# Kernel optimization log

Measured on AMD Instinct MI355X. Metric: run time of the kernel, lower is better.

The kernel has to match this reference:

```python
import jax, jax.numpy as jnp
import numpy as np

B, T, C, H = 65536, 100, 7, 2  # batch, timesteps, covariates, lstm hidden


def setup_inputs() -> dict:
    key = jax.random.key(0)
    ks = iter(jax.random.split(key, 32))
    def rn(shape, s=0.1):
        return jax.random.normal(next(ks), shape, dtype=jnp.float32) * s
    inp = {"x": jax.random.normal(next(ks), (B, T, C), dtype=jnp.float32)}
    for l, din in ((0, C), (1, 2 * H)):
        for suf in ("", "r"):
            inp[f"w_ih_l{l}{suf}"] = rn((4 * H, din))
            inp[f"w_hh_l{l}{suf}"] = rn((4 * H, H))
            inp[f"b_ih_l{l}{suf}"] = rn((4 * H,))
            inp[f"b_hh_l{l}{suf}"] = rn((4 * H,))
    inp["fc1_w"] = rn((64, 4 * T))
    inp["fc1_b"] = rn((64,))
    inp["fc2_w"] = rn((20, 64))
    inp["fc2_b"] = rn((20,))
    return inp


def _lstm_dir(xw, w_hh, b_hh, reverse):
    # xw: [T, B, 4H] precomputed input projection (x @ W_ih.T + b_ih)
    if reverse:
        xw = xw[::-1]
    h0 = jnp.zeros((xw.shape[1], H), xw.dtype)
    c0 = jnp.zeros((xw.shape[1], H), xw.dtype)

    def step(carry, gx):
        h, c = carry
        g = gx + h @ w_hh.T + b_hh            # [B, 4H]
        i, f, gg, o = jnp.split(g, 4, axis=-1)  # torch gate order i,f,g,o
        c = jax.nn.sigmoid(f) * c + jax.nn.sigmoid(i) * jnp.tanh(gg)
        h = jax.nn.sigmoid(o) * jnp.tanh(c)
        return (h, c), h

    _, hs = jax.lax.scan(step, (h0, c0), xw)
    if reverse:
        hs = hs[::-1]
    return hs  # [T, B, H]


def _bilstm_layer(x_tbf, w_ih_f, w_hh_f, b_ih_f, b_hh_f,
                  w_ih_b, w_hh_b, b_ih_b, b_hh_b):
    xw_f = jnp.einsum('tbc,gc->tbg', x_tbf, w_ih_f) + b_ih_f
    xw_b = jnp.einsum('tbc,gc->tbg', x_tbf, w_ih_b) + b_ih_b
    hf = _lstm_dir(xw_f, w_hh_f, b_hh_f, False)
    hb = _lstm_dir(xw_b, w_hh_b, b_hh_b, True)
    return jnp.concatenate([hf, hb], axis=-1)  # [T, B, 2H]


def reference(x,
              w_ih_l0, w_hh_l0, b_ih_l0, b_hh_l0,
              w_ih_l0r, w_hh_l0r, b_ih_l0r, b_hh_l0r,
              w_ih_l1, w_hh_l1, b_ih_l1, b_hh_l1,
              w_ih_l1r, w_hh_l1r, b_ih_l1r, b_hh_l1r,
              fc1_w, fc1_b, fc2_w, fc2_b):
    xt = jnp.transpose(x.reshape(-1, T, C), (1, 0, 2))  # [T, B, C] time-major
    h1 = _bilstm_layer(xt, w_ih_l0, w_hh_l0, b_ih_l0, b_hh_l0,
                       w_ih_l0r, w_hh_l0r, b_ih_l0r, b_hh_l0r)
    h2 = _bilstm_layer(h1, w_ih_l1, w_hh_l1, b_ih_l1, b_hh_l1,
                       w_ih_l1r, w_hh_l1r, b_ih_l1r, b_hh_l1r)
    out = jnp.transpose(h2, (1, 0, 2)).reshape(-1, 4 * T)  # flatten [B, 4T]
    out = jax.nn.relu(out)                  # relu BEFORE fc1, as in original
    out = jax.nn.relu(out @ fc1_w.T + fc1_b)
    return out @ fc2_w.T + fc2_b            # [B, 20]
```

## Files before the change

### kernel.cpp

```cpp
#include <hip/hip_runtime.h>

#define Bn 65536
#define Tn 100
#define Cn 7

typedef short short8 __attribute__((ext_vector_type(8)));
typedef float float4v __attribute__((ext_vector_type(4)));

__device__ __forceinline__ float fast_rcp(float x) { return __builtin_amdgcn_rcpf(x); }
__device__ __forceinline__ float sig_f(float x) { return fast_rcp(1.f + __expf(-x)); }
__device__ __forceinline__ float tanh_f(float x) { return 1.f - 2.f * fast_rcp(__expf(2.f * x) + 1.f); }
__device__ __forceinline__ unsigned bf16rne(float x) {
    unsigned u = __float_as_uint(x);
    return (u + 0x7fffu + ((u >> 16) & 1u)) >> 16;
}
__device__ __forceinline__ float bf_lo(unsigned u) { return __uint_as_float(u << 16); }
__device__ __forceinline__ float bf_hi(unsigned u) { return __uint_as_float(u & 0xffff0000u); }

__device__ __forceinline__ float dpp_xor1(float x) {
    return __uint_as_float((unsigned)__builtin_amdgcn_mov_dpp(
        (int)__float_as_uint(x), 0xB1, 0xF, 0xF, true));
}

typedef const __attribute__((address_space(1))) void* gp_t;
typedef __attribute__((address_space(3))) void* sp_t;
__device__ __forceinline__ void async_copy_dw(const void* g, void* l) {
    __builtin_amdgcn_global_load_lds((gp_t)g, (sp_t)l, 4, 0, 0);
}

__global__ void w2prep_kernel(const float* __restrict__ fc1_w, unsigned short* __restrict__ w2g) {
    int idx = blockIdx.x * 256 + threadIdx.x;
    int w  = idx >> 12;
    int d  = (idx >> 11) & 1;
    int n  = (idx >> 5) & 63;
    int kk = idx & 31;
    int tt = kk >> 1, i = kk & 1;
    int t  = d ? (99 - 10 * w - tt) : (10 * w + tt);
    float v = (kk < 20) ? fc1_w[n * 400 + 4 * t + 2 * d + i] : 0.f;
    w2g[idx] = (unsigned short)bf16rne(v);
}

__global__ __launch_bounds__(256) void l0_kernel(
    const float* __restrict__ x,
    const float* __restrict__ wih_f, const float* __restrict__ whh_f,
    const float* __restrict__ bih_f, const float* __restrict__ bhh_f,
    const float* __restrict__ wih_r, const float* __restrict__ whh_r,
    const float* __restrict__ bih_r, const float* __restrict__ bhh_r,
    unsigned* __restrict__ h1u)
{
    __shared__ float xs[4][2][1120];

    const int tid  = threadIdx.x;
    const int wv   = tid >> 6;
    const int lane = tid & 63;
    const int rev  = wv >> 1;
    const int sgrp = wv & 1;
    const int cid  = lane & 1;
    const int s    = lane >> 1;
    const int b    = blockIdx.x * 64 + sgrp * 32 + s;

    const float* wih = rev ? wih_r : wih_f;
    const float* whh = rev ? whh_r : whh_f;
    const float* bih = rev ? bih_r : bih_f;
    const float* bhh = rev ? bhh_r : bhh_f;

    float wi[28], whA[4], whB[4], bias4[4];
#pragma unroll
    for (int j = 0; j < 4; ++j) {
        const int k = cid + 2 * j;
#pragma unroll
        for (int c = 0; c < 7; ++c) wi[j * 7 + c] = wih[k * 7 + c];
        whA[j] = whh[k * 2 + cid];
        whB[j] = whh[k * 2 + (cid ^ 1)];
        bias4[j] = bih[k] + bhh[k];
    }

    const int e  = (lane >= 35) ? 1 : 0;
    const int r0 = lane - 35 * e;
    const float* xsamp = x + (size_t)(blockIdx.x * 64 + sgrp * 32 + e) * 700;

    auto stage = [&](int ch, int p) {
        const int off = rev ? (665 - 35 * ch) : (35 * ch);
        const float* g = xsamp + off + r0;
        float* l = &xs[wv][p][lane];
        int r = r0;
#pragma unroll
        for (int i = 0; i < 17; ++i) {
            async_copy_dw(g, l);
            l += 64;
            const int c = (r >= 6) ? 1 : 0;
            g += c ? 1394 : 729;
            r += c ? -6 : 29;
        }
        if (lane < 32) async_copy_dw(g, l);
    };

    float hs = 0.f, ho = 0.f, cc = 0.f;

    stage(0, 0);
#pragma unroll 1
    for (int chk = 0; chk < 20; ++chk) {
        if (chk == 0) __builtin_amdgcn_s_waitcnt(0x0F70);
        else          __builtin_amdgcn_s_waitcnt(0x0F75);
        __builtin_amdgcn_sched_barrier(0);
        if (chk < 19) stage(chk + 1, (chk + 1) & 1);
        __builtin_amdgcn_sched_barrier(0);

        const int t0 = rev ? (95 - 5 * chk) : (5 * chk);
        const float* xbuf = &xs[wv][chk & 1][0];
#pragma unroll
        for (int tt = 0; tt < 5; ++tt) {
            const int rr = rev ? (4 - tt) : tt;
            const int t  = t0 + rr;
            const float* xrow = xbuf + s * 35 + rr * 7;

            float g[4];
#pragma unroll
            for (int j = 0; j < 4; ++j) g[j] = bias4[j];
#pragma unroll
            for (int c = 0; c < 7; ++c) {
                const float xv = xrow[c];
#pragma unroll
                for (int j = 0; j < 4; ++j) g[j] = fmaf(wi[j * 7 + c], xv, g[j]);
            }
#pragma unroll
            for (int j = 0; j < 4; ++j)
                g[j] = fmaf(whA[j], hs, fmaf(whB[j], ho, g[j]));

            const float iv = sig_f(g[0]);
            const float fv = sig_f(g[1]);
            const float qv = tanh_f(g[2]);
            const float ov = sig_f(g[3]);
            cc = fmaf(fv, cc, iv * qv);
            hs = ov * tanh_f(cc);
            ho = dpp_xor1(hs);

            if (cid == 0)
                h1u[((size_t)t * 2 + rev) * Bn + b] = bf16rne(hs) | (bf16rne(ho) << 16);
        }
    }
}

__global__ __launch_bounds__(256) void l1fc_kernel(
    const unsigned* __restrict__ hin,
    const float* __restrict__ wih_f, const float* __restrict__ whh_f,
    const float* __restrict__ bih_f, const float* __restrict__ bhh_f,
    const float* __restrict__ wih_r, const float* __restrict__ whh_r,
    const float* __restrict__ bih_r, const float* __restrict__ bhh_r,
    const unsigned* __restrict__ w2g,
    const float* __restrict__ fc1_b,
    const float* __restrict__ fc2_w,
    const float* __restrict__ fc2_b,
    float* __restrict__ out)
{
    __shared__ unsigned smem[11776];
    unsigned* a2  = smem;
    unsigned* w2b = smem + 2560;
    unsigned* hst = smem + 6656;

    const int tid  = threadIdx.x;
    const int wv   = tid >> 6;
    const int lane = tid & 63;
    const int d    = tid >> 7;
    const int cid  = tid & 1;
    const int s    = (tid & 127) >> 1;
    const int b0   = blockIdx.x * 64;

    const float* wih = d ? wih_r : wih_f;
    const float* whh = d ? whh_r : whh_f;
    const float* bih = d ? bih_r : bih_f;
    const float* bhh = d ? bhh_r : bhh_f;

    float wi[16], whA[4], whB[4], bias4[4];
#pragma unroll
    for (int j = 0; j < 4; ++j) {
        const int k = cid + 2 * j;
#pragma unroll
        for (int m = 0; m < 4; ++m) wi[j * 4 + m] = wih[k * 4 + m];
        whA[j] = whh[k * 2 + cid];
        whB[j] = whh[k * 2 + (cid ^ 1)];
        bias4[j] = bih[k] + bhh[k];
    }

    float4v acc[4];
#pragma unroll
    for (int nt = 0; nt < 4; ++nt) acc[nt] = (float4v){0.f, 0.f, 0.f, 0.f};

    for (int i = tid; i < 2560; i += 256) a2[i] = 0u;

    auto stage_h = [&](int w, int pb) {
        unsigned* dst = hst + pb * 2560;
        const int Rb = tid >> 6;
        const int s2 = tid & 63;
#pragma unroll
        for (int i = 0; i < 10; ++i) {
            const int R  = Rb + 4 * i;
            const int dd = (R >= 20) ? 1 : 0;
            const int r2 = R - 20 * dd;
            const int p  = (r2 >= 10) ? 1 : 0;
            const int j  = r2 - 10 * p;
            const int t  = dd ? (99 - (10 * w + j)) : (10 * w + j);
            async_copy_dw(hin + ((size_t)t * 2 + p) * Bn + b0 + s2, dst + R * 64 + s2);
        }
    };
    auto stage_w = [&](int w, int pb) {
        const unsigned* src = w2g + w * 2048;
        unsigned* dst = w2b + pb * 2048;
#pragma unroll
        for (int i = 0; i < 8; ++i)
            async_copy_dw(src + i * 256 + tid, dst + i * 256 + tid);
    };

    stage_h(0, 0); stage_w(0, 0);

    float hs = 0.f, ho = 0.f, cc = 0.f;
    const int q = lane >> 4, l16 = lane & 15;

#pragma unroll 1
    for (int w = 0; w < 10; ++w) {
        __builtin_amdgcn_s_waitcnt(0x0F70);
        __syncthreads();
        if (w < 9) { stage_h(w + 1, (w + 1) & 1); stage_w(w + 1, (w + 1) & 1); }

        const unsigned* hb = hst + (w & 1) * 2560 + d * 1280;
#pragma unroll 2
        for (int j = 0; j < 10; ++j) {
            const unsigned uF = hb[j * 64 + s];
            const unsigned uR = hb[640 + j * 64 + s];
            const float aF0 = bf_lo(uF), aF1 = bf_hi(uF);
            const float aR0 = bf_lo(uR), aR1 = bf_hi(uR);

            float g[4];
#pragma unroll
            for (int jj = 0; jj < 4; ++jj) {
                g[jj] = bias4[jj];
                g[jj] = fmaf(wi[jj * 4 + 0], aF0, g[jj]);
                g[jj] = fmaf(wi[jj * 4 + 1], aF1, g[jj]);
                g[jj] = fmaf(wi[jj * 4 + 2], aR0, g[jj]);
                g[jj] = fmaf(wi[jj * 4 + 3], aR1, g[jj]);
                g[jj] = fmaf(whA[jj], hs, fmaf(whB[jj], ho, g[jj]));
            }
            const float iv = sig_f(g[0]);
            const float fv = sig_f(g[1]);
            const float qv = tanh_f(g[2]);
            const float ov = sig_f(g[3]);
            cc = fmaf(fv, cc, iv * qv);
            hs = ov * tanh_f(cc);
            ho = dpp_xor1(hs);

            if (cid == 0)
                a2[d * 1280 + s * 20 + j] =
                    bf16rne(fmaxf(hs, 0.f)) | (bf16rne(fmaxf(ho, 0.f)) << 16);
        }
        __syncthreads();

        {
            const unsigned* wb = w2b + (w & 1) * 2048;
#pragma unroll
            for (int dd = 0; dd < 2; ++dd) {
                short8 av = *(const short8*)&a2[dd * 1280 + (wv * 16 + l16) * 20 + q * 4];
                short8 bv[4];
#pragma unroll
                for (int nt = 0; nt < 4; ++nt)
                    bv[nt] = *(const short8*)&wb[dd * 1024 + (nt * 16 + l16) * 16 + q * 4];
#pragma unroll
                for (int nt = 0; nt < 4; ++nt)
                    acc[nt] = __builtin_amdgcn_mfma_f32_16x16x32_bf16(
                        av, bv[nt], acc[nt], 0, 0, 0);
            }
        }
    }
    __syncthreads();

    {
        float* eb = (float*)smem;
#pragma unroll
        for (int nt = 0; nt < 4; ++nt)
#pragma unroll
            for (int r = 0; r < 4; ++r) {
                const int sl = wv * 16 + q * 4 + r;
                const int cl = nt * 16 + l16;
                eb[sl * 65 + cl] = acc[nt][r];
            }
    }
    __syncthreads();

    const float* eb = (const float*)smem;
    const int sm2 = tid & 63;
    const int og  = (tid >> 6) * 5;
    float z[64];
#pragma unroll
    for (int k = 0; k < 64; ++k) z[k] = fmaxf(eb[sm2 * 65 + k] + fc1_b[k], 0.f);
    float y[5];
#pragma unroll
    for (int o = 0; o < 5; ++o) {
        float r2 = fc2_b[og + o];
#pragma unroll
        for (int k = 0; k < 64; ++k) r2 = fmaf(fc2_w[(og + o) * 64 + k], z[k], r2);
        y[o] = r2;
    }
    __syncthreads();
    float* ebw = (float*)smem;
#pragma unroll
    for (int o = 0; o < 5; ++o) ebw[sm2 * 20 + og + o] = y[o];
    __syncthreads();
    for (int f = tid; f < 1280; f += 256)
        out[(size_t)blockIdx.x * 1280 + f] = ebw[f];
}

extern "C" void kernel_launch(void* const* d_in, const int* in_sizes, int n_in,
                              void* d_out, int out_size, void* d_ws, size_t ws_size,
                              hipStream_t stream) {
    const float* x = (const float*)d_in[0];
    const float* w_ih_l0  = (const float*)d_in[1];
    const float* w_hh_l0  = (const float*)d_in[2];
    const float* b_ih_l0  = (const float*)d_in[3];
    const float* b_hh_l0  = (const float*)d_in[4];
    const float* w_ih_l0r = (const float*)d_in[5];
    const float* w_hh_l0r = (const float*)d_in[6];
    const float* b_ih_l0r = (const float*)d_in[7];
    const float* b_hh_l0r = (const float*)d_in[8];
    const float* w_ih_l1  = (const float*)d_in[9];
    const float* w_hh_l1  = (const float*)d_in[10];
    const float* b_ih_l1  = (const float*)d_in[11];
    const float* b_hh_l1  = (const float*)d_in[12];
    const float* w_ih_l1r = (const float*)d_in[13];
    const float* w_hh_l1r = (const float*)d_in[14];
    const float* b_ih_l1r = (const float*)d_in[15];
    const float* b_hh_l1r = (const float*)d_in[16];
    const float* fc1_w = (const float*)d_in[17];
    const float* fc1_b = (const float*)d_in[18];
    const float* fc2_w = (const float*)d_in[19];
    const float* fc2_b = (const float*)d_in[20];

    unsigned* h1u = (unsigned*)d_ws;
    unsigned short* w2g = (unsigned short*)((char*)d_ws + (size_t)Tn * 2 * Bn * 4);

    w2prep_kernel<<<160, 256, 0, stream>>>(fc1_w, w2g);
    l0_kernel<<<1024, 256, 0, stream>>>(x,
        w_ih_l0, w_hh_l0, b_ih_l0, b_hh_l0,
        w_ih_l0r, w_hh_l0r, b_ih_l0r, b_hh_l0r, h1u);
    l1fc_kernel<<<1024, 256, 0, stream>>>(h1u,
        w_ih_l1, w_hh_l1, b_ih_l1, b_hh_l1,
        w_ih_l1r, w_hh_l1r, b_ih_l1r, b_hh_l1r,
        (const unsigned*)w2g, fc1_b, fc2_w, fc2_b, (float*)d_out);
}
```

Before: 414.9 us.

## Use packed FMA in LSTM gates and make layer-1 waves independent without block barriers

Both LSTM kernels now compute gate pre-activations with packed two-wide FMAs, which cuts VALU instruction count. The layer-0 kernel stages two timesteps per chunk instead of five, which shrinks LDS use so more blocks fit per CU, and it adds an occupancy launch bound. The layer-1 kernel gives each wave its own 32-sample, single-direction slice with private LDS buffers. fc1 weights are read straight from global memory into registers, so the per-window __syncthreads are gone, and the forward and reverse partial accumulators are summed in LDS at the end. In exchange there are more chunk iterations and waitcnts, and fc1 weight fragments are loaded redundantly from global/L2.

```diff
diff --git a/kernel.cpp b/kernel.cpp
--- a/kernel.cpp
+++ b/kernel.cpp
@@ -6,6 +6,12 @@
 
 typedef short short8 __attribute__((ext_vector_type(8)));
 typedef float float4v __attribute__((ext_vector_type(4)));
+typedef float float2v __attribute__((ext_vector_type(2)));
+
+__device__ __forceinline__ float2v pk_fma(float2v a, float2v b, float2v c) {
+    return __builtin_elementwise_fma(a, b, c);
+}
+__device__ __forceinline__ float2v pk2(float v) { return (float2v){v, v}; }
 
 __device__ __forceinline__ float fast_rcp(float x) { return __builtin_amdgcn_rcpf(x); }
 __device__ __forceinline__ float sig_f(float x) { return fast_rcp(1.f + __expf(-x)); }
@@ -40,7 +46,7 @@
     w2g[idx] = (unsigned short)bf16rne(v);
 }
 
-__global__ __launch_bounds__(256) void l0_kernel(
+__global__ __launch_bounds__(256, 8) void l0_kernel(
     const float* __restrict__ x,
     const float* __restrict__ wih_f, const float* __restrict__ whh_f,
     const float* __restrict__ bih_f, const float* __restrict__ bhh_f,
@@ -48,7 +54,7 @@
     const float* __restrict__ bih_r, const float* __restrict__ bhh_r,
     unsigned* __restrict__ h1u)
 {
-    __shared__ float xs[4][2][1120];
+    __shared__ float xs[4][2][448];
 
     const int tid  = threadIdx.x;
     const int wv   = tid >> 6;
@@ -64,73 +70,70 @@
     const float* bih = rev ? bih_r : bih_f;
     const float* bhh = rev ? bhh_r : bhh_f;
 
-    float wi[28], whA[4], whB[4], bias4[4];
-#pragma unroll
-    for (int j = 0; j < 4; ++j) {
-        const int k = cid + 2 * j;
-#pragma unroll
-        for (int c = 0; c < 7; ++c) wi[j * 7 + c] = wih[k * 7 + c];
-        whA[j] = whh[k * 2 + cid];
-        whB[j] = whh[k * 2 + (cid ^ 1)];
-        bias4[j] = bih[k] + bhh[k];
-    }
-
-    const int e  = (lane >= 35) ? 1 : 0;
-    const int r0 = lane - 35 * e;
-    const float* xsamp = x + (size_t)(blockIdx.x * 64 + sgrp * 32 + e) * 700;
+    float2v wi2[2][7], whA2[2], whB2[2], bias2[2];
+#pragma unroll
+    for (int p = 0; p < 2; ++p) {
+        const int k0 = cid + 4 * p, k1 = cid + 4 * p + 2;
+#pragma unroll
+        for (int c = 0; c < 7; ++c)
+            wi2[p][c] = (float2v){wih[k0 * 7 + c], wih[k1 * 7 + c]};
+        whA2[p]  = (float2v){whh[k0 * 2 + cid], whh[k1 * 2 + cid]};
+        whB2[p]  = (float2v){whh[k0 * 2 + (cid ^ 1)], whh[k1 * 2 + (cid ^ 1)]};
+        bias2[p] = (float2v){bih[k0] + bhh[k0], bih[k1] + bhh[k1]};
+    }
+
+    const int s0 = lane / 14;
+    const int r0 = lane - 14 * s0;
+    const float* xsamp = x + (size_t)(blockIdx.x * 64 + sgrp * 32 + s0) * 700;
 
     auto stage = [&](int ch, int p) {
-        const int off = rev ? (665 - 35 * ch) : (35 * ch);
+        const int off = rev ? (686 - 14 * ch) : (14 * ch);
         const float* g = xsamp + off + r0;
         float* l = &xs[wv][p][lane];
         int r = r0;
 #pragma unroll
-        for (int i = 0; i < 17; ++i) {
+        for (int i = 0; i < 7; ++i) {
             async_copy_dw(g, l);
             l += 64;
             const int c = (r >= 6) ? 1 : 0;
-            g += c ? 1394 : 729;
-            r += c ? -6 : 29;
-        }
-        if (lane < 32) async_copy_dw(g, l);
+            g += c ? 3494 : 2808;
+            r += c ? -6 : 8;
+        }
     };
 
     float hs = 0.f, ho = 0.f, cc = 0.f;
 
     stage(0, 0);
 #pragma unroll 1
-    for (int chk = 0; chk < 20; ++chk) {
+    for (int chk = 0; chk < 50; ++chk) {
         if (chk == 0) __builtin_amdgcn_s_waitcnt(0x0F70);
-        else          __builtin_amdgcn_s_waitcnt(0x0F75);
-        __builtin_amdgcn_sched_barrier(0);
-        if (chk < 19) stage(chk + 1, (chk + 1) & 1);
-        __builtin_amdgcn_sched_barrier(0);
-
-        const int t0 = rev ? (95 - 5 * chk) : (5 * chk);
+        else          __builtin_amdgcn_s_waitcnt(0x0F72);
+        __builtin_amdgcn_sched_barrier(0);
+        if (chk < 49) stage(chk + 1, (chk + 1) & 1);
+        __builtin_amdgcn_sched_barrier(0);
+
+        const int t0 = rev ? (98 - 2 * chk) : (2 * chk);
         const float* xbuf = &xs[wv][chk & 1][0];
 #pragma unroll
-        for (int tt = 0; tt < 5; ++tt) {
-            const int rr = rev ? (4 - tt) : tt;
+        for (int tt = 0; tt < 2; ++tt) {
+            const int rr = rev ? (1 - tt) : tt;
             const int t  = t0 + rr;
-            const float* xrow = xbuf + s * 35 + rr * 7;
-
-            float g[4];
-#pragma unroll
-            for (int j = 0; j < 4; ++j) g[j] = bias4[j];
+            const float* xrow = xbuf + s * 14 + rr * 7;
+
+            float2v g0 = bias2[0], g1 = bias2[1];
 #pragma unroll
             for (int c = 0; c < 7; ++c) {
                 const float xv = xrow[c];
-#pragma unroll
-                for (int j = 0; j < 4; ++j) g[j] = fmaf(wi[j * 7 + c], xv, g[j]);
+                g0 = pk_fma(wi2[0][c], pk2(xv), g0);
+                g1 = pk_fma(wi2[1][c], pk2(xv), g1);
             }
-#pragma unroll
-            for (int j = 0; j < 4; ++j)
-                g[j] = fmaf(whA[j], hs, fmaf(whB[j], ho, g[j]));
-
-            const float iv = sig_f(g[0]);
-            const float fv = sig_f(g[1]);
-            const float qv = tanh_f(g[2]);
-            const float ov = sig_f(g[3]);
+            g0 = pk_fma(whA2[0], pk2(hs), pk_fma(whB2[0], pk2(ho), g0));
+            g1 = pk_fma(whA2[1], pk2(hs), pk_fma(whB2[1], pk2(ho), g1));
+
+            const float iv = sig_f(g0.x);
+            const float fv = sig_f(g0.y);
+            const float qv = tanh_f(g1.x);
+            const float ov = sig_f(g1.y);
             cc = fmaf(fv, cc, iv * qv);
             hs = ov * tanh_f(cc);
             ho = dpp_xor1(hs);
@@ -141,7 +144,7 @@
     }
 }
 
-__global__ __launch_bounds__(256) void l1fc_kernel(
+__global__ __launch_bounds__(256, 4) void l1fc_kernel(
     const unsigned* __restrict__ hin,
     const float* __restrict__ wih_f, const float* __restrict__ whh_f,
     const float* __restrict__ bih_f, const float* __restrict__ bhh_f,
@@ -153,65 +156,61 @@
     const float* __restrict__ fc2_b,
     float* __restrict__ out)
 {
-    __shared__ unsigned smem[11776];
-    unsigned* a2  = smem;
-    unsigned* w2b = smem + 2560;
-    unsigned* hst = smem + 6656;
+    __shared__ unsigned smem[7680];
 
     const int tid  = threadIdx.x;
     const int wv   = tid >> 6;
     const int lane = tid & 63;
-    const int d    = tid >> 7;
-    const int cid  = tid & 1;
-    const int s    = (tid & 127) >> 1;
+    const int d    = wv >> 1;
+    const int shalf = wv & 1;
+    const int cid  = lane & 1;
+    const int sp   = lane >> 1;
     const int b0   = blockIdx.x * 64;
+
+    unsigned* a2w  = smem + wv * 640;
+    unsigned* hstw = smem + 2560 + wv * 1280;
 
     const float* wih = d ? wih_r : wih_f;
     const float* whh = d ? whh_r : whh_f;
     const float* bih = d ? bih_r : bih_f;
     const float* bhh = d ? bhh_r : bhh_f;
 
-    float wi[16], whA[4], whB[4], bias4[4];
-#pragma unroll
-    for (int j = 0; j < 4; ++j) {
-        const int k = cid + 2 * j;
-#pragma unroll
-        for (int m = 0; m < 4; ++m) wi[j * 4 + m] = wih[k * 4 + m];
-        whA[j] = whh[k * 2 + cid];
-        whB[j] = whh[k * 2 + (cid ^ 1)];
-        bias4[j] = bih[k] + bhh[k];
-    }
-
-    float4v acc[4];
-#pragma unroll
-    for (int nt = 0; nt < 4; ++nt) acc[nt] = (float4v){0.f, 0.f, 0.f, 0.f};
-
-    for (int i = tid; i < 2560; i += 256) a2[i] = 0u;
+    float2v wi2[2][4], whA2[2], whB2[2], bias2[2];
+#pragma unroll
+    for (int p = 0; p < 2; ++p) {
+        const int k0 = cid + 4 * p, k1 = cid + 4 * p + 2;
+#pragma unroll
+        for (int m = 0; m < 4; ++m)
+            wi2[p][m] = (float2v){wih[k0 * 4 + m], wih[k1 * 4 + m]};
+        whA2[p]  = (float2v){whh[k0 * 2 + cid], whh[k1 * 2 + cid]};
+        whB2[p]  = (float2v){whh[k0 * 2 + (cid ^ 1)], whh[k1 * 2 + (cid ^ 1)]};
+        bias2[p] = (float2v){bih[k0] + bhh[k0], bih[k1] + bhh[k1]};
+    }
+
+    float4v acc[2][4];
+#pragma unroll
+    for (int mt = 0; mt < 2; ++mt)
+#pragma unroll
+        for (int nt = 0; nt < 4; ++nt) acc[mt][nt] = (float4v){0.f, 0.f, 0.f, 0.f};
+
+    for (int i = lane; i < 640; i += 64) a2w[i] = 0u;
 
     auto stage_h = [&](int w, int pb) {
-        unsigned* dst = hst + pb * 2560;
-        const int Rb = tid >> 6;
-        const int s2 = tid & 63;
+        unsigned* dst = hstw + pb * 640;
+        const int col = lane & 31;
+        const int Rb  = lane >> 5;
 #pragma unroll
         for (int i = 0; i < 10; ++i) {
-            const int R  = Rb + 4 * i;
-            const int dd = (R >= 20) ? 1 : 0;
-            const int r2 = R - 20 * dd;
-            const int p  = (r2 >= 10) ? 1 : 0;
-            const int j  = r2 - 10 * p;
-            const int t  = dd ? (99 - (10 * w + j)) : (10 * w + j);
-            async_copy_dw(hin + ((size_t)t * 2 + p) * Bn + b0 + s2, dst + R * 64 + s2);
+            const int R = Rb + 2 * i;
+            const int p = (R >= 10) ? 1 : 0;
+            const int j = R - 10 * p;
+            const int t = d ? (99 - (10 * w + j)) : (10 * w + j);
+            async_copy_dw(hin + ((size_t)t * 2 + p) * Bn + b0 + shalf * 32 + col,
+                          dst + R * 32 + col);
         }
     };
-    auto stage_w = [&](int w, int pb) {
-        const unsigned* src = w2g + w * 2048;
-        unsigned* dst = w2b + pb * 2048;
-#pragma unroll
-        for (int i = 0; i < 8; ++i)
-            async_copy_dw(src + i * 256 + tid, dst + i * 256 + tid);
-    };
-
-    stage_h(0, 0); stage_w(0, 0);
+
+    stage_h(0, 0);
 
     float hs = 0.f, ho = 0.f, cc = 0.f;
     const int q = lane >> 4, l16 = lane & 15;
@@ -219,78 +218,86 @@
 #pragma unroll 1
     for (int w = 0; w < 10; ++w) {
         __builtin_amdgcn_s_waitcnt(0x0F70);
-        __syncthreads();
-        if (w < 9) { stage_h(w + 1, (w + 1) & 1); stage_w(w + 1, (w + 1) & 1); }
-
-        const unsigned* hb = hst + (w & 1) * 2560 + d * 1280;
+        __builtin_amdgcn_sched_barrier(0);
+
+        short8 bv[4];
+#pragma unroll
+        for (int nt = 0; nt < 4; ++nt)
+            bv[nt] = *(const short8*)&w2g[w * 2048 + d * 1024 + (nt * 16 + l16) * 16 + q * 4];
+
+        if (w < 9) stage_h(w + 1, (w + 1) & 1);
+        __builtin_amdgcn_sched_barrier(0);
+
+        const unsigned* hb = hstw + (w & 1) * 640;
 #pragma unroll 2
         for (int j = 0; j < 10; ++j) {
-            const unsigned uF = hb[j * 64 + s];
-            const unsigned uR = hb[640 + j * 64 + s];
-            const float aF0 = bf_lo(uF), aF1 = bf_hi(uF);
-            const float aR0 = bf_lo(uR), aR1 = bf_hi(uR);
-
-            float g[4];
-#pragma unroll
-            for (int jj = 0; jj < 4; ++jj) {
-                g[jj] = bias4[jj];
-                g[jj] = fmaf(wi[jj * 4 + 0], aF0, g[jj]);
-                g[jj] = fmaf(wi[jj * 4 + 1], aF1, g[jj]);
-                g[jj] = fmaf(wi[jj * 4 + 2], aR0, g[jj]);
-                g[jj] = fmaf(wi[jj * 4 + 3], aR1, g[jj]);
-                g[jj] = fmaf(whA[jj], hs, fmaf(whB[jj], ho, g[jj]));
-            }
-            const float iv = sig_f(g[0]);
-            const float fv = sig_f(g[1]);
-            const float qv = tanh_f(g[2]);
-            const float ov = sig_f(g[3]);
+            const unsigned uF = hb[j * 32 + sp];
+            const unsigned uR = hb[320 + j * 32 + sp];
+            const float a0 = bf_lo(uF), a1 = bf_hi(uF);
+            const float a2v = bf_lo(uR), a3 = bf_hi(uR);
+
+            float2v g0 = bias2[0], g1 = bias2[1];
+            g0 = pk_fma(wi2[0][0], pk2(a0), g0);  g1 = pk_fma(wi2[1][0], pk2(a0), g1);
+            g0 = pk_fma(wi2[0][1], pk2(a1), g0);  g1 = pk_fma(wi2[1][1], pk2(a1), g1);
+            g0 = pk_fma(wi2[0][2], pk2(a2v), g0); g1 = pk_fma(wi2[1][2], pk2(a2v), g1);
+            g0 = pk_fma(wi2[0][3], pk2(a3), g0);  g1 = pk_fma(wi2[1][3], pk2(a3), g1);
+            g0 = pk_fma(whA2[0], pk2(hs), pk_fma(whB2[0], pk2(ho), g0));
+            g1 = pk_fma(whA2[1], pk2(hs), pk_fma(whB2[1], pk2(ho), g1));
+
+            const float iv = sig_f(g0.x);
+            const float fv = sig_f(g0.y);
+            const float qv = tanh_f(g1.x);
+            const float ov = sig_f(g1.y);
             cc = fmaf(fv, cc, iv * qv);
             hs = ov * tanh_f(cc);
             ho = dpp_xor1(hs);
 
             if (cid == 0)
-                a2[d * 1280 + s * 20 + j] =
-                    bf16rne(fmaxf(hs, 0.f)) | (bf16rne(fmaxf(ho, 0.f)) << 16);
-        }
-        __syncthreads();
+                a2w[sp * 20 + j] = bf16rne(fmaxf(hs, 0.f)) | (bf16rne(fmaxf(ho, 0.f)) << 16);
+        }
+        asm volatile("s_waitcnt lgkmcnt(0)");
+        __builtin_amdgcn_sched_barrier(0);
 
         {
-            const unsigned* wb = w2b + (w & 1) * 2048;
-#pragma unroll
-            for (int dd = 0; dd < 2; ++dd) {
-                short8 av = *(const short8*)&a2[dd * 1280 + (wv * 16 + l16) * 20 + q * 4];
-                short8 bv[4];
-#pragma unroll
-                for (int nt = 0; nt < 4; ++nt)
-                    bv[nt] = *(const short8*)&wb[dd * 1024 + (nt * 16 + l16) * 16 + q * 4];
-#pragma unroll
-                for (int nt = 0; nt < 4; ++nt)
-                    acc[nt] = __builtin_amdgcn_mfma_f32_16x16x32_bf16(
-                        av, bv[nt], acc[nt], 0, 0, 0);
+            short8 av0 = *(const short8*)&a2w[l16 * 20 + q * 4];
+            short8 av1 = *(const short8*)&a2w[(16 + l16) * 20 + q * 4];
+#pragma unroll
+            for (int nt = 0; nt < 4; ++nt) {
+                acc[0][nt] = __builtin_amdgcn_mfma_f32_16x16x32_bf16(av0, bv[nt], acc[0][nt], 0, 0, 0);
+                acc[1][nt] = __builtin_amdgcn_mfma_f32_16x16x32_bf16(av1, bv[nt], acc[1][nt], 0, 0, 0);
             }
         }
     }
-    __syncthreads();
-
-    {
-        float* eb = (float*)smem;
-#pragma unroll
-        for (int nt = 0; nt < 4; ++nt)
-#pragma unroll
-            for (int r = 0; r < 4; ++r) {
-                const int sl = wv * 16 + q * 4 + r;
-                const int cl = nt * 16 + l16;
-                eb[sl * 65 + cl] = acc[nt][r];
-            }
-    }
-    __syncthreads();
-
-    const float* eb = (const float*)smem;
+
+    __syncthreads();
+    float* eb = (float*)smem;
+    if (d == 0) {
+#pragma unroll
+        for (int mt = 0; mt < 2; ++mt)
+#pragma unroll
+            for (int nt = 0; nt < 4; ++nt)
+#pragma unroll
+                for (int r = 0; r < 4; ++r)
+                    eb[(shalf * 32 + mt * 16 + q * 4 + r) * 65 + nt * 16 + l16] = acc[mt][nt][r];
+    }
+    __syncthreads();
+    if (d == 1) {
+#pragma unroll
+        for (int mt = 0; mt < 2; ++mt)
+#pragma unroll
+            for (int nt = 0; nt < 4; ++nt)
+#pragma unroll
+                for (int r = 0; r < 4; ++r)
+                    eb[(shalf * 32 + mt * 16 + q * 4 + r) * 65 + nt * 16 + l16] += acc[mt][nt][r];
+    }
+    __syncthreads();
+
+    const float* ebr = (const float*)smem;
     const int sm2 = tid & 63;
     const int og  = (tid >> 6) * 5;
     float z[64];
 #pragma unroll
-    for (int k = 0; k < 64; ++k) z[k] = fmaxf(eb[sm2 * 65 + k] + fc1_b[k], 0.f);
+    for (int k = 0; k < 64; ++k) z[k] = fmaxf(ebr[sm2 * 65 + k] + fc1_b[k], 0.f);
     float y[5];
 #pragma unroll
     for (int o = 0; o < 5; ++o) {
```

New measurement: 490.3 us. 18.2% more time.
